# Kernel tuning notes

Hardware: AMD Instinct MI355X
Metric: run time of the kernel (lower is better)

## Reference

```python
import jax, jax.numpy as jnp
import numpy as np

N_NODES = 50000
N_EDGES = 1600000
D_IN = 128
D_OUT = 32
N_HEADS = 4


def setup_inputs() -> dict:
    key = jax.random.key(0)
    k1, k2, k3, k4 = jax.random.split(key, 4)
    x = jax.random.normal(k1, (N_NODES, D_IN), dtype=jnp.float32)
    edge_index = jax.random.randint(k2, (2, N_EDGES), 0, N_NODES, dtype=jnp.int64)
    W = jax.random.normal(k3, (N_HEADS, D_IN, D_OUT), dtype=jnp.float32) * 0.01
    a = jax.random.normal(k4, (N_HEADS, 2 * D_OUT), dtype=jnp.float32) * 0.01
    return {"x": x, "edge_index": edge_index, "W": W, "a": a}


def reference(x, edge_index, W, a):
    N = x.shape[0]
    K, d_in, d_out = W.shape
    # Per-head projected node features: [N, K, d_out]
    Wh = jnp.einsum('ni,kio->nko', x, W)
    src, tgt = edge_index[0], edge_index[1]
    # cat([Wh[src], Wh[tgt]]) . a  ==  Wh[src].a[:, :d] + Wh[tgt].a[:, d:]
    s_src = jnp.einsum('nkd,kd->nk', Wh, a[:, :d_out])  # [N, K]
    s_tgt = jnp.einsum('nkd,kd->nk', Wh, a[:, d_out:])  # [N, K]
    e = s_src[src] + s_tgt[tgt]                          # [E, K]
    e = jnp.where(e > 0, e, 0.2 * e)                     # LeakyReLU(0.2)
    # Segment-softmax over incoming edges of each target node
    e_max = jax.ops.segment_max(e, tgt, num_segments=N)  # [N, K], -inf for empty
    e_max = jnp.where(jnp.isfinite(e_max), e_max, 0.0)
    e_exp = jnp.exp(e - e_max[tgt])                      # [E, K]
    e_sum = jax.ops.segment_sum(e_exp, tgt, num_segments=N)  # [N, K]
    alpha = e_exp / (e_sum[tgt] + 1e-10)                 # [E, K]
    # Weighted scatter-add aggregation: [N, K, d_out]
    weighted = alpha[:, :, None] * Wh[src]
    out = jax.ops.segment_sum(weighted, tgt, num_segments=N)
    out = out.reshape(N, K * d_out)
    return jnp.where(out > 0, out, jnp.expm1(out))       # ELU
```

## Files before the change

### kernel.cpp

```cpp
#include <hip/hip_runtime.h>
#include <math.h>

#define N_HEADS 4
#define D_IN    128
#define D_OUT   32
#define D_TOT   128
#define TN      64
#define XPAD    132
#define BSH     6
#define BNODES  64
#define MAXNB   1024
#define EPT     16
#define CAP     2816

static __device__ __forceinline__ unsigned short f2bf(float f) {
    unsigned u = __float_as_uint(f);
    u += 0x7fffu + ((u >> 16) & 1u);
    return (unsigned short)(u >> 16);
}

__global__ __launch_bounds__(256) void front_kernel(
    const float* __restrict__ x,
    const float* __restrict__ W,
    const float* __restrict__ a,
    const int*  __restrict__ ei,
    int*  __restrict__ cursor,
    unsigned int* __restrict__ bbuf,
    unsigned int* __restrict__ Whu,
    float* __restrict__ s_src,
    float* __restrict__ s_tgt,
    int N, int E, int nProj, int nb) {

    __shared__ float xs[TN][XPAD];
    const int t = threadIdx.x;

    if (blockIdx.x >= nProj) {
        int* cnt = (int*)xs;
        for (int i = t; i < nb; i += 256) cnt[i] = 0;
        __syncthreads();

        const int e0 = (blockIdx.x - nProj) * (256 * EPT);
        int src[EPT], tgt[EPT];
        #pragma unroll
        for (int i = 0; i < EPT; ++i) {
            int e = e0 + i * 256 + t;
            if (e < E) {
                src[i] = ei[e];
                tgt[i] = ei[E + e];
                atomicAdd(&cnt[tgt[i] >> BSH], 1);
            } else {
                src[i] = -1; tgt[i] = 0;
            }
        }
        __syncthreads();
        for (int b = t; b < nb; b += 256)
            if (cnt[b]) cnt[b] = atomicAdd(&cursor[b], cnt[b]);
        __syncthreads();
        #pragma unroll
        for (int i = 0; i < EPT; ++i) {
            if (src[i] >= 0) {
                int b = tgt[i] >> BSH;
                int pos = atomicAdd(&cnt[b], 1);
                if (pos < CAP)
                    bbuf[(size_t)b * CAP + pos] =
                        ((unsigned)(tgt[i] & (BNODES - 1)) << 16) | (unsigned)src[i];
            }
        }
        return;
    }

    const int n0 = blockIdx.x * TN;
    {
        const int r  = t >> 2;
        const int c0 = (t & 3) * 32;
        int nn = n0 + r; if (nn >= N) nn = N - 1;
        const float4* src = (const float4*)(x + (size_t)nn * D_IN + c0);
        #pragma unroll
        for (int j = 0; j < 8; ++j)
            *(float4*)&xs[r][c0 + j * 4] = src[j];
    }
    __syncthreads();

    const int fg = t & 15;
    const int ng = t >> 4;
    const int f0 = fg * 8;
    const int k  = f0 >> 5;
    const int o0 = f0 & 31;
    const float* Wf = W + k * (D_IN * D_OUT) + o0;

    float acc[4][8];
    #pragma unroll
    for (int nl = 0; nl < 4; ++nl)
        #pragma unroll
        for (int j = 0; j < 8; ++j) acc[nl][j] = 0.f;

    #pragma unroll 2
    for (int i = 0; i < D_IN; i += 4) {
        float4 wa[4], wb[4];
        #pragma unroll
        for (int ii = 0; ii < 4; ++ii) {
            wa[ii] = *(const float4*)(Wf + (i + ii) * D_OUT);
            wb[ii] = *(const float4*)(Wf + (i + ii) * D_OUT + 4);
        }
        #pragma unroll
        for (int nl = 0; nl < 4; ++nl) {
            const float4 xv = *(const float4*)&xs[ng * 4 + nl][i];
            const float xr[4] = {xv.x, xv.y, xv.z, xv.w};
            #pragma unroll
            for (int ii = 0; ii < 4; ++ii) {
                acc[nl][0] = fmaf(xr[ii], wa[ii].x, acc[nl][0]);
                acc[nl][1] = fmaf(xr[ii], wa[ii].y, acc[nl][1]);
                acc[nl][2] = fmaf(xr[ii], wa[ii].z, acc[nl][2]);
                acc[nl][3] = fmaf(xr[ii], wa[ii].w, acc[nl][3]);
                acc[nl][4] = fmaf(xr[ii], wb[ii].x, acc[nl][4]);
                acc[nl][5] = fmaf(xr[ii], wb[ii].y, acc[nl][5]);
                acc[nl][6] = fmaf(xr[ii], wb[ii].z, acc[nl][6]);
                acc[nl][7] = fmaf(xr[ii], wb[ii].w, acc[nl][7]);
            }
        }
    }

    const float4 as0 = *(const float4*)(a + k * (2 * D_OUT) + o0);
    const float4 as1 = *(const float4*)(a + k * (2 * D_OUT) + o0 + 4);
    const float4 at0 = *(const float4*)(a + k * (2 * D_OUT) + D_OUT + o0);
    const float4 at1 = *(const float4*)(a + k * (2 * D_OUT) + D_OUT + o0 + 4);

    #pragma unroll
    for (int nl = 0; nl < 4; ++nl) {
        const int n = n0 + ng * 4 + nl;
        if (n < N) {
            unsigned int p[4];
            #pragma unroll
            for (int j = 0; j < 4; ++j)
                p[j] = (unsigned)f2bf(acc[nl][2 * j]) |
                       ((unsigned)f2bf(acc[nl][2 * j + 1]) << 16);
            *(uint4*)&Whu[(size_t)n * 64 + fg * 4] = make_uint4(p[0], p[1], p[2], p[3]);

            float vs = acc[nl][0] * as0.x + acc[nl][1] * as0.y +
                       acc[nl][2] * as0.z + acc[nl][3] * as0.w +
                       acc[nl][4] * as1.x + acc[nl][5] * as1.y +
                       acc[nl][6] * as1.z + acc[nl][7] * as1.w;
            float vt = acc[nl][0] * at0.x + acc[nl][1] * at0.y +
                       acc[nl][2] * at0.z + acc[nl][3] * at0.w +
                       acc[nl][4] * at1.x + acc[nl][5] * at1.y +
                       acc[nl][6] * at1.z + acc[nl][7] * at1.w;
            vs += __shfl_xor(vs, 1, 64); vs += __shfl_xor(vs, 2, 64);
            vt += __shfl_xor(vt, 1, 64); vt += __shfl_xor(vt, 2, 64);
            if ((fg & 3) == 0) {
                s_src[n * N_HEADS + k] = vs;
                s_tgt[n * N_HEADS + k] = vt;
            }
        }
    }
}

__global__ __launch_bounds__(256) void finalize_kernel(
    const unsigned int* __restrict__ bbuf,
    const int* __restrict__ cursor,
    int* __restrict__ rs_beg,
    int* __restrict__ rs_end,
    unsigned short* __restrict__ rec,
    int N) {

    __shared__ int hist[BNODES];
    __shared__ int cur[BNODES];
    const int b = blockIdx.x;
    const int t = threadIdx.x;
    const int cnt = cursor[b];
    const int base = b * CAP;

    if (t < BNODES) hist[t] = 0;
    __syncthreads();
    for (int j = t; j < cnt; j += 256)
        atomicAdd(&hist[bbuf[base + j] >> 16], 1);
    __syncthreads();

    if (t < BNODES) {
        int v = hist[t];
        int vp = (v + 7) & ~7;
        int incl = vp;
        #pragma unroll
        for (int off = 1; off < 64; off <<= 1) {
            int tv = __shfl_up(incl, off, 64);
            if (t >= off) incl += tv;
        }
        int excl = incl - vp;
        if (excl > CAP) excl = CAP;
        int e2 = excl + v;
        if (e2 > CAP) e2 = CAP;
        cur[t] = excl;
        int n = b * BNODES + t;
        if (n < N) {
            rs_beg[n] = base + excl;
            rs_end[n] = base + e2;
        }
    }
    __syncthreads();

    for (int j = t; j < cnt; j += 256) {
        unsigned v = bbuf[base + j];
        int pos = atomicAdd(&cur[v >> 16], 1);
        if (pos < CAP)
            rec[base + pos] = (unsigned short)(v & 0xFFFFu);
    }
}

__global__ __launch_bounds__(256) void agg_kernel(
    const unsigned short* __restrict__ rec,
    const int* __restrict__ rs_beg,
    const int* __restrict__ rs_end,
    const float* __restrict__ s_src,
    const float* __restrict__ s_tgt,
    const unsigned int* __restrict__ Whu,
    float* __restrict__ out, int N) {

    __shared__ float evs[4][64];
    const int wid = threadIdx.x >> 6;
    const int n = blockIdx.x * 4 + wid;
    if (n >= N) return;
    const int t   = threadIdx.x & 63;
    const int k   = t >> 4;
    const int i16 = t & 15;

    const int beg = rs_beg[n];
    const int end = rs_end[n];
    const float stk = s_tgt[((size_t)n << 2) + k];
    const uint4* rec128 = (const uint4*)rec;

    float denp = 0.f, nx = 0.f, ny = 0.f;
    for (int j = beg; j < end; j += 16) {
        const uint4 da = rec128[(unsigned)(j >> 3)];
        const uint4 db = rec128[(unsigned)(j >> 3) + 1];
        const int own = j + i16;
        const unsigned svo = rec[own];
        const float ssv = s_src[((size_t)svo << 2) + k];
        float av = ssv + stk;
        av = fmaxf(av, 0.2f * av);
        const float evv = (own < end) ? __expf(av) : 0.f;
        denp += evv;
        evs[wid][t] = evv;

        int sv[16];
        sv[0]  = (int)(da.x & 0xffffu); sv[1]  = (int)(da.x >> 16);
        sv[2]  = (int)(da.y & 0xffffu); sv[3]  = (int)(da.y >> 16);
        sv[4]  = (int)(da.z & 0xffffu); sv[5]  = (int)(da.z >> 16);
        sv[6]  = (int)(da.w & 0xffffu); sv[7]  = (int)(da.w >> 16);
        sv[8]  = (int)(db.x & 0xffffu); sv[9]  = (int)(db.x >> 16);
        sv[10] = (int)(db.y & 0xffffu); sv[11] = (int)(db.y >> 16);
        sv[12] = (int)(db.z & 0xffffu); sv[13] = (int)(db.z >> 16);
        sv[14] = (int)(db.w & 0xffffu); sv[15] = (int)(db.w >> 16);

        unsigned w[16];
        #pragma unroll
        for (int q = 0; q < 16; ++q)
            w[q] = Whu[((unsigned)sv[q] << 6) + (unsigned)t];

        float e[16];
        *(float4*)&e[0]  = *(const float4*)&evs[wid][(k << 4) + 0];
        *(float4*)&e[4]  = *(const float4*)&evs[wid][(k << 4) + 4];
        *(float4*)&e[8]  = *(const float4*)&evs[wid][(k << 4) + 8];
        *(float4*)&e[12] = *(const float4*)&evs[wid][(k << 4) + 12];

        #pragma unroll
        for (int q = 0; q < 16; ++q) {
            nx = fmaf(e[q], __uint_as_float(w[q] << 16), nx);
            ny = fmaf(e[q], __uint_as_float(w[q] & 0xffff0000u), ny);
        }
    }

    denp += __shfl_xor(denp, 1, 64);
    denp += __shfl_xor(denp, 2, 64);
    denp += __shfl_xor(denp, 4, 64);
    denp += __shfl_xor(denp, 8, 64);

    const float inv = 1.f / (denp + 1e-10f);
    float ox = nx * inv, oy = ny * inv;
    ox = ox > 0.f ? ox : expm1f(ox);
    oy = oy > 0.f ? oy : expm1f(oy);
    *(float2*)&out[((size_t)n << 7) + (t << 1)] = make_float2(ox, oy);
}

extern "C" void kernel_launch(void* const* d_in, const int* in_sizes, int n_in,
                              void* d_out, int out_size, void* d_ws, size_t ws_size,
                              hipStream_t stream) {
    const float* x  = (const float*)d_in[0];
    const int*   ei = (const int*)d_in[1];
    const float* W  = (const float*)d_in[2];
    const float* a  = (const float*)d_in[3];
    float* out = (float*)d_out;

    const int N = in_sizes[0] / D_IN;
    const int E = in_sizes[1] / 2;
    const int nb = (N + BNODES - 1) >> BSH;

    char* p = (char*)d_ws;
    auto align256 = [](size_t v) { return (v + 255) & ~(size_t)255; };
    unsigned int* Whu = (unsigned int*)p;      p += align256((size_t)N * 64 * 4);
    float* s_src    = (float*)p;               p += align256((size_t)N * N_HEADS * 4);
    float* s_tgt    = (float*)p;               p += align256((size_t)N * N_HEADS * 4);
    int*   cursor   = (int*)p;                 p += align256((size_t)nb * 4);
    int*   rs_beg   = (int*)p;                 p += align256((size_t)N * 4);
    int*   rs_end   = (int*)p;                 p += align256((size_t)N * 4);
    unsigned int* bbuf = (unsigned int*)p;     p += align256((size_t)nb * CAP * 4);
    unsigned short* rec = (unsigned short*)p;

    hipMemsetAsync(cursor, 0, (size_t)nb * sizeof(int), stream);

    const int nProj = (N + TN - 1) / TN;
    const int nBkt  = (E + 256 * EPT - 1) / (256 * EPT);
    front_kernel<<<nProj + nBkt, 256, 0, stream>>>(
        x, W, a, ei, cursor, bbuf, Whu, s_src, s_tgt, N, E, nProj, nb);

    finalize_kernel<<<nb, 256, 0, stream>>>(bbuf, cursor, rs_beg, rs_end, rec, N);

    agg_kernel<<<(N + 3) / 4, 256, 0, stream>>>(
        rec, rs_beg, rs_end, s_src, s_tgt, Whu, out, N);
}
```

Measured before the change: 122.7 us.

## Replace bucketed CSR build with fixed-capacity per-node slots via global atomics

Drops the two-level bucket sort (block-local histogram, bucket buffer, finalize kernel) and instead has each edge do a global atomicAdd on a per-node cursor, writing its source id into a fixed 80-slot row per target node. The aggregation kernel reads the count from the cursor and walks the node's fixed slot range. This removes one kernel launch and the intermediate bucket buffer pass. In exchange it adds 1.6M contended global atomics, scattered 2-byte writes, and a larger memset of the slot array. Any edges past 80 per node are silently dropped.

```diff
diff --git a/kernel.cpp b/kernel.cpp
--- a/kernel.cpp
+++ b/kernel.cpp
@@ -4,14 +4,10 @@
 #define N_HEADS 4
 #define D_IN    128
 #define D_OUT   32
-#define D_TOT   128
 #define TN      64
 #define XPAD    132
-#define BSH     6
-#define BNODES  64
-#define MAXNB   1024
 #define EPT     16
-#define CAP     2816
+#define NCAP    80
 
 static __device__ __forceinline__ unsigned short f2bf(float f) {
     unsigned u = __float_as_uint(f);
@@ -25,45 +21,26 @@
     const float* __restrict__ a,
     const int*  __restrict__ ei,
     int*  __restrict__ cursor,
-    unsigned int* __restrict__ bbuf,
+    unsigned short* __restrict__ rec,
     unsigned int* __restrict__ Whu,
     float* __restrict__ s_src,
     float* __restrict__ s_tgt,
-    int N, int E, int nProj, int nb) {
+    int N, int E, int nProj) {
 
     __shared__ float xs[TN][XPAD];
     const int t = threadIdx.x;
 
     if (blockIdx.x >= nProj) {
-        int* cnt = (int*)xs;
-        for (int i = t; i < nb; i += 256) cnt[i] = 0;
-        __syncthreads();
-
         const int e0 = (blockIdx.x - nProj) * (256 * EPT);
-        int src[EPT], tgt[EPT];
         #pragma unroll
         for (int i = 0; i < EPT; ++i) {
             int e = e0 + i * 256 + t;
             if (e < E) {
-                src[i] = ei[e];
-                tgt[i] = ei[E + e];
-                atomicAdd(&cnt[tgt[i] >> BSH], 1);
-            } else {
-                src[i] = -1; tgt[i] = 0;
-            }
-        }
-        __syncthreads();
-        for (int b = t; b < nb; b += 256)
-            if (cnt[b]) cnt[b] = atomicAdd(&cursor[b], cnt[b]);
-        __syncthreads();
-        #pragma unroll
-        for (int i = 0; i < EPT; ++i) {
-            if (src[i] >= 0) {
-                int b = tgt[i] >> BSH;
-                int pos = atomicAdd(&cnt[b], 1);
-                if (pos < CAP)
-                    bbuf[(size_t)b * CAP + pos] =
-                        ((unsigned)(tgt[i] & (BNODES - 1)) << 16) | (unsigned)src[i];
+                int s = ei[e];
+                int g = ei[E + e];
+                int pos = atomicAdd(&cursor[g], 1);
+                if (pos < NCAP)
+                    rec[(size_t)g * NCAP + pos] = (unsigned short)s;
             }
         }
         return;
@@ -154,61 +131,9 @@
     }
 }
 
-__global__ __launch_bounds__(256) void finalize_kernel(
-    const unsigned int* __restrict__ bbuf,
-    const int* __restrict__ cursor,
-    int* __restrict__ rs_beg,
-    int* __restrict__ rs_end,
-    unsigned short* __restrict__ rec,
-    int N) {
-
-    __shared__ int hist[BNODES];
-    __shared__ int cur[BNODES];
-    const int b = blockIdx.x;
-    const int t = threadIdx.x;
-    const int cnt = cursor[b];
-    const int base = b * CAP;
-
-    if (t < BNODES) hist[t] = 0;
-    __syncthreads();
-    for (int j = t; j < cnt; j += 256)
-        atomicAdd(&hist[bbuf[base + j] >> 16], 1);
-    __syncthreads();
-
-    if (t < BNODES) {
-        int v = hist[t];
-        int vp = (v + 7) & ~7;
-        int incl = vp;
-        #pragma unroll
-        for (int off = 1; off < 64; off <<= 1) {
-            int tv = __shfl_up(incl, off, 64);
-            if (t >= off) incl += tv;
-        }
-        int excl = incl - vp;
-        if (excl > CAP) excl = CAP;
-        int e2 = excl + v;
-        if (e2 > CAP) e2 = CAP;
-        cur[t] = excl;
-        int n = b * BNODES + t;
-        if (n < N) {
-            rs_beg[n] = base + excl;
-            rs_end[n] = base + e2;
-        }
-    }
-    __syncthreads();
-
-    for (int j = t; j < cnt; j += 256) {
-        unsigned v = bbuf[base + j];
-        int pos = atomicAdd(&cur[v >> 16], 1);
-        if (pos < CAP)
-            rec[base + pos] = (unsigned short)(v & 0xFFFFu);
-    }
-}
-
 __global__ __launch_bounds__(256) void agg_kernel(
     const unsigned short* __restrict__ rec,
-    const int* __restrict__ rs_beg,
-    const int* __restrict__ rs_end,
+    const int* __restrict__ cursor,
     const float* __restrict__ s_src,
     const float* __restrict__ s_tgt,
     const unsigned int* __restrict__ Whu,
@@ -222,15 +147,15 @@
     const int k   = t >> 4;
     const int i16 = t & 15;
 
-    const int beg = rs_beg[n];
-    const int end = rs_end[n];
+    const int cnt = cursor[n];
+    const int beg = n * NCAP;
+    const int end = beg + (cnt < NCAP ? cnt : NCAP);
     const float stk = s_tgt[((size_t)n << 2) + k];
-    const uint4* rec128 = (const uint4*)rec;
 
     float denp = 0.f, nx = 0.f, ny = 0.f;
     for (int j = beg; j < end; j += 16) {
-        const uint4 da = rec128[(unsigned)(j >> 3)];
-        const uint4 db = rec128[(unsigned)(j >> 3) + 1];
+        const uint4 da = *(const uint4*)(rec + j);
+        const uint4 db = *(const uint4*)(rec + j + 8);
         const int own = j + i16;
         const unsigned svo = rec[own];
         const float ssv = s_src[((size_t)svo << 2) + k];
@@ -291,28 +216,23 @@
 
     const int N = in_sizes[0] / D_IN;
     const int E = in_sizes[1] / 2;
-    const int nb = (N + BNODES - 1) >> BSH;
 
     char* p = (char*)d_ws;
     auto align256 = [](size_t v) { return (v + 255) & ~(size_t)255; };
     unsigned int* Whu = (unsigned int*)p;      p += align256((size_t)N * 64 * 4);
     float* s_src    = (float*)p;               p += align256((size_t)N * N_HEADS * 4);
     float* s_tgt    = (float*)p;               p += align256((size_t)N * N_HEADS * 4);
-    int*   cursor   = (int*)p;                 p += align256((size_t)nb * 4);
-    int*   rs_beg   = (int*)p;                 p += align256((size_t)N * 4);
-    int*   rs_end   = (int*)p;                 p += align256((size_t)N * 4);
-    unsigned int* bbuf = (unsigned int*)p;     p += align256((size_t)nb * CAP * 4);
+    const size_t curBytes = align256((size_t)N * 4);
+    int*   cursor   = (int*)p;                 p += curBytes;
     unsigned short* rec = (unsigned short*)p;
 
-    hipMemsetAsync(cursor, 0, (size_t)nb * sizeof(int), stream);
+    hipMemsetAsync(cursor, 0, curBytes + (size_t)N * NCAP * 2, stream);
 
     const int nProj = (N + TN - 1) / TN;
     const int nBkt  = (E + 256 * EPT - 1) / (256 * EPT);
     front_kernel<<<nProj + nBkt, 256, 0, stream>>>(
-        x, W, a, ei, cursor, bbuf, Whu, s_src, s_tgt, N, E, nProj, nb);
-
-    finalize_kernel<<<nb, 256, 0, stream>>>(bbuf, cursor, rs_beg, rs_end, rec, N);
+        x, W, a, ei, cursor, rec, Whu, s_src, s_tgt, N, E, nProj);
 
     agg_kernel<<<(N + 3) / 4, 256, 0, stream>>>(
-        rec, rs_beg, rs_end, s_src, s_tgt, Whu, out, N);
-}
+        rec, cursor, s_src, s_tgt, Whu, out, N);
+}
```

Measured after the change: 168.6 us. 37.4% more time.

## Fuse bucket finalize and aggregation into one per-bucket kernel with LDS ordering

Applied to the files above, without the earlier changes.

Merges the finalize (counting sort per 64-node bucket) and aggregation kernels into a single kernel. Each block loads its bucket into shared memory, sorts the source ids there, and eight waves then aggregate the 64 nodes straight from shared memory. This removes one launch and the global write/read of the sorted record array and the row start/end arrays. In exchange, parallelism drops to about 782 blocks of 512 threads with heavy LDS use, so load imbalance and occupancy may suffer. CAP is reduced to 2560 and per-bucket counts are clipped, which raises the risk of silently dropping edges in dense buckets.

```diff
diff --git a/kernel.cpp b/kernel.cpp
--- a/kernel.cpp
+++ b/kernel.cpp
@@ -4,14 +4,15 @@
 #define N_HEADS 4
 #define D_IN    128
 #define D_OUT   32
-#define D_TOT   128
 #define TN      64
 #define XPAD    132
 #define BSH     6
 #define BNODES  64
-#define MAXNB   1024
 #define EPT     16
-#define CAP     2816
+#define CAP     2560
+#define BT      512
+#define NW      8
+#define ORD     3072
 
 static __device__ __forceinline__ unsigned short f2bf(float f) {
     unsigned u = __float_as_uint(f);
@@ -154,130 +155,125 @@
     }
 }
 
-__global__ __launch_bounds__(256) void finalize_kernel(
+__global__ __launch_bounds__(BT) void bagg_kernel(
     const unsigned int* __restrict__ bbuf,
     const int* __restrict__ cursor,
-    int* __restrict__ rs_beg,
-    int* __restrict__ rs_end,
-    unsigned short* __restrict__ rec,
-    int N) {
-
-    __shared__ int hist[BNODES];
-    __shared__ int cur[BNODES];
-    const int b = blockIdx.x;
-    const int t = threadIdx.x;
-    const int cnt = cursor[b];
-    const int base = b * CAP;
-
-    if (t < BNODES) hist[t] = 0;
-    __syncthreads();
-    for (int j = t; j < cnt; j += 256)
-        atomicAdd(&hist[bbuf[base + j] >> 16], 1);
-    __syncthreads();
-
-    if (t < BNODES) {
-        int v = hist[t];
-        int vp = (v + 7) & ~7;
-        int incl = vp;
-        #pragma unroll
-        for (int off = 1; off < 64; off <<= 1) {
-            int tv = __shfl_up(incl, off, 64);
-            if (t >= off) incl += tv;
-        }
-        int excl = incl - vp;
-        if (excl > CAP) excl = CAP;
-        int e2 = excl + v;
-        if (e2 > CAP) e2 = CAP;
-        cur[t] = excl;
-        int n = b * BNODES + t;
-        if (n < N) {
-            rs_beg[n] = base + excl;
-            rs_end[n] = base + e2;
-        }
-    }
-    __syncthreads();
-
-    for (int j = t; j < cnt; j += 256) {
-        unsigned v = bbuf[base + j];
-        int pos = atomicAdd(&cur[v >> 16], 1);
-        if (pos < CAP)
-            rec[base + pos] = (unsigned short)(v & 0xFFFFu);
-    }
-}
-
-__global__ __launch_bounds__(256) void agg_kernel(
-    const unsigned short* __restrict__ rec,
-    const int* __restrict__ rs_beg,
-    const int* __restrict__ rs_end,
     const float* __restrict__ s_src,
     const float* __restrict__ s_tgt,
     const unsigned int* __restrict__ Whu,
     float* __restrict__ out, int N) {
 
-    __shared__ float evs[4][64];
-    const int wid = threadIdx.x >> 6;
-    const int n = blockIdx.x * 4 + wid;
-    if (n >= N) return;
-    const int t   = threadIdx.x & 63;
+    __shared__ unsigned stg[CAP];
+    __shared__ __align__(16) unsigned short ord[ORD];
+    __shared__ int hist[BNODES], cur[BNODES];
+    __shared__ int begs[BNODES], ends[BNODES];
+    __shared__ float evs[NW][64];
+
+    const int b   = blockIdx.x;
+    const int tt  = threadIdx.x;
+    const int wid = tt >> 6;
+    const int t   = tt & 63;
     const int k   = t >> 4;
     const int i16 = t & 15;
 
-    const int beg = rs_beg[n];
-    const int end = rs_end[n];
-    const float stk = s_tgt[((size_t)n << 2) + k];
-    const uint4* rec128 = (const uint4*)rec;
-
-    float denp = 0.f, nx = 0.f, ny = 0.f;
-    for (int j = beg; j < end; j += 16) {
-        const uint4 da = rec128[(unsigned)(j >> 3)];
-        const uint4 db = rec128[(unsigned)(j >> 3) + 1];
-        const int own = j + i16;
-        const unsigned svo = rec[own];
-        const float ssv = s_src[((size_t)svo << 2) + k];
-        float av = ssv + stk;
-        av = fmaxf(av, 0.2f * av);
-        const float evv = (own < end) ? __expf(av) : 0.f;
-        denp += evv;
-        evs[wid][t] = evv;
-
-        int sv[16];
-        sv[0]  = (int)(da.x & 0xffffu); sv[1]  = (int)(da.x >> 16);
-        sv[2]  = (int)(da.y & 0xffffu); sv[3]  = (int)(da.y >> 16);
-        sv[4]  = (int)(da.z & 0xffffu); sv[5]  = (int)(da.z >> 16);
-        sv[6]  = (int)(da.w & 0xffffu); sv[7]  = (int)(da.w >> 16);
-        sv[8]  = (int)(db.x & 0xffffu); sv[9]  = (int)(db.x >> 16);
-        sv[10] = (int)(db.y & 0xffffu); sv[11] = (int)(db.y >> 16);
-        sv[12] = (int)(db.z & 0xffffu); sv[13] = (int)(db.z >> 16);
-        sv[14] = (int)(db.w & 0xffffu); sv[15] = (int)(db.w >> 16);
-
-        unsigned w[16];
-        #pragma unroll
-        for (int q = 0; q < 16; ++q)
-            w[q] = Whu[((unsigned)sv[q] << 6) + (unsigned)t];
-
-        float e[16];
-        *(float4*)&e[0]  = *(const float4*)&evs[wid][(k << 4) + 0];
-        *(float4*)&e[4]  = *(const float4*)&evs[wid][(k << 4) + 4];
-        *(float4*)&e[8]  = *(const float4*)&evs[wid][(k << 4) + 8];
-        *(float4*)&e[12] = *(const float4*)&evs[wid][(k << 4) + 12];
-
-        #pragma unroll
-        for (int q = 0; q < 16; ++q) {
-            nx = fmaf(e[q], __uint_as_float(w[q] << 16), nx);
-            ny = fmaf(e[q], __uint_as_float(w[q] & 0xffff0000u), ny);
-        }
-    }
-
-    denp += __shfl_xor(denp, 1, 64);
-    denp += __shfl_xor(denp, 2, 64);
-    denp += __shfl_xor(denp, 4, 64);
-    denp += __shfl_xor(denp, 8, 64);
-
-    const float inv = 1.f / (denp + 1e-10f);
-    float ox = nx * inv, oy = ny * inv;
-    ox = ox > 0.f ? ox : expm1f(ox);
-    oy = oy > 0.f ? oy : expm1f(oy);
-    *(float2*)&out[((size_t)n << 7) + (t << 1)] = make_float2(ox, oy);
+    if (tt < BNODES) hist[tt] = 0;
+    for (int i = tt; i < ORD / 2; i += BT) ((unsigned*)ord)[i] = 0;
+    __syncthreads();
+
+    int cnt = cursor[b]; if (cnt > CAP) cnt = CAP;
+    const unsigned* bbp = bbuf + (size_t)b * CAP;
+    for (int i = tt; i < cnt; i += BT) {
+        unsigned v = bbp[i];
+        stg[i] = v;
+        atomicAdd(&hist[v >> 16], 1);
+    }
+    __syncthreads();
+
+    if (tt < BNODES) {
+        int v = hist[tt];
+        int vp = (v + 7) & ~7;
+        int incl = vp;
+        #pragma unroll
+        for (int off = 1; off < 64; off <<= 1) {
+            int tv = __shfl_up(incl, off, 64);
+            if (tt >= off) incl += tv;
+        }
+        int excl = incl - vp;
+        cur[tt]  = excl;
+        begs[tt] = excl;
+        ends[tt] = excl + v;
+    }
+    __syncthreads();
+
+    for (int i = tt; i < cnt; i += BT) {
+        unsigned v = stg[i];
+        int pos = atomicAdd(&cur[v >> 16], 1);
+        ord[pos] = (unsigned short)(v & 0xffffu);
+    }
+    __syncthreads();
+
+    #pragma unroll
+    for (int r2 = 0; r2 < BNODES / NW; ++r2) {
+        const int ln  = (wid << 3) + r2;
+        const int n   = b * BNODES + ln;
+        const int beg = begs[ln];
+        const int end = ends[ln];
+        const float stk = s_tgt[((size_t)n << 2) + k];
+
+        float denp = 0.f, nx = 0.f, ny = 0.f;
+        for (int j = beg; j < end; j += 16) {
+            const uint4 da = *(const uint4*)&ord[j];
+            const uint4 db = *(const uint4*)&ord[j + 8];
+            const int own = j + i16;
+            const unsigned svo = ord[own];
+            const float ssv = s_src[((size_t)svo << 2) + k];
+            float av = ssv + stk;
+            av = fmaxf(av, 0.2f * av);
+            const float evv = (own < end) ? __expf(av) : 0.f;
+            denp += evv;
+            evs[wid][t] = evv;
+
+            int sv[16];
+            sv[0]  = (int)(da.x & 0xffffu); sv[1]  = (int)(da.x >> 16);
+            sv[2]  = (int)(da.y & 0xffffu); sv[3]  = (int)(da.y >> 16);
+            sv[4]  = (int)(da.z & 0xffffu); sv[5]  = (int)(da.z >> 16);
+            sv[6]  = (int)(da.w & 0xffffu); sv[7]  = (int)(da.w >> 16);
+            sv[8]  = (int)(db.x & 0xffffu); sv[9]  = (int)(db.x >> 16);
+            sv[10] = (int)(db.y & 0xffffu); sv[11] = (int)(db.y >> 16);
+            sv[12] = (int)(db.z & 0xffffu); sv[13] = (int)(db.z >> 16);
+            sv[14] = (int)(db.w & 0xffffu); sv[15] = (int)(db.w >> 16);
+
+            unsigned w[16];
+            #pragma unroll
+            for (int q = 0; q < 16; ++q)
+                w[q] = Whu[((unsigned)sv[q] << 6) + (unsigned)t];
+
+            float e[16];
+            *(float4*)&e[0]  = *(const float4*)&evs[wid][(k << 4) + 0];
+            *(float4*)&e[4]  = *(const float4*)&evs[wid][(k << 4) + 4];
+            *(float4*)&e[8]  = *(const float4*)&evs[wid][(k << 4) + 8];
+            *(float4*)&e[12] = *(const float4*)&evs[wid][(k << 4) + 12];
+
+            #pragma unroll
+            for (int q = 0; q < 16; ++q) {
+                nx = fmaf(e[q], __uint_as_float(w[q] << 16), nx);
+                ny = fmaf(e[q], __uint_as_float(w[q] & 0xffff0000u), ny);
+            }
+        }
+
+        denp += __shfl_xor(denp, 1, 64);
+        denp += __shfl_xor(denp, 2, 64);
+        denp += __shfl_xor(denp, 4, 64);
+        denp += __shfl_xor(denp, 8, 64);
+
+        if (n < N) {
+            const float inv = 1.f / (denp + 1e-10f);
+            float ox = nx * inv, oy = ny * inv;
+            ox = ox > 0.f ? ox : expm1f(ox);
+            oy = oy > 0.f ? oy : expm1f(oy);
+            *(float2*)&out[((size_t)n << 7) + (t << 1)] = make_float2(ox, oy);
+        }
+    }
 }
 
 extern "C" void kernel_launch(void* const* d_in, const int* in_sizes, int n_in,
@@ -298,21 +294,17 @@
     unsigned int* Whu = (unsigned int*)p;      p += align256((size_t)N * 64 * 4);
     float* s_src    = (float*)p;               p += align256((size_t)N * N_HEADS * 4);
     float* s_tgt    = (float*)p;               p += align256((size_t)N * N_HEADS * 4);
-    int*   cursor   = (int*)p;                 p += align256((size_t)nb * 4);
-    int*   rs_beg   = (int*)p;                 p += align256((size_t)N * 4);
-    int*   rs_end   = (int*)p;                 p += align256((size_t)N * 4);
-    unsigned int* bbuf = (unsigned int*)p;     p += align256((size_t)nb * CAP * 4);
-    unsigned short* rec = (unsigned short*)p;
-
-    hipMemsetAsync(cursor, 0, (size_t)nb * sizeof(int), stream);
+    const size_t curBytes = align256((size_t)nb * 4);
+    int*   cursor   = (int*)p;                 p += curBytes;
+    unsigned int* bbuf = (unsigned int*)p;
+
+    hipMemsetAsync(cursor, 0, curBytes, stream);
 
     const int nProj = (N + TN - 1) / TN;
     const int nBkt  = (E + 256 * EPT - 1) / (256 * EPT);
     front_kernel<<<nProj + nBkt, 256, 0, stream>>>(
         x, W, a, ei, cursor, bbuf, Whu, s_src, s_tgt, N, E, nProj, nb);
 
-    finalize_kernel<<<nb, 256, 0, stream>>>(bbuf, cursor, rs_beg, rs_end, rec, N);
-
-    agg_kernel<<<(N + 3) / 4, 256, 0, stream>>>(
-        rec, rs_beg, rs_end, s_src, s_tgt, Whu, out, N);
+    bagg_kernel<<<nb, BT, 0, stream>>>(
+        bbuf, cursor, s_src, s_tgt, Whu, out, N);
 }
```

Measured after the change: 123.9 us. About the same (+1.0%).
